# Optimization experiments

Hardware: AMD Instinct MI355X
Metric: run time of the kernel (lower is better)

## Reference

```python
import jax, jax.numpy as jnp
import numpy as np

HEADS = 12
DIM_HEAD = 64
WINDOW = 16
SHIFT = 1  # fixed stand-in for random.randint(0, window-1)
SCALE = DIM_HEAD ** -0.5


def window_cls_mask(n, window, shift):
    # Shifted block-diagonal mask over the n-1 non-CLS tokens, CLS attends/attended everywhere.
    size = n - 1
    idx = jnp.arange(size)
    cur = (idx - shift) % window
    left = jnp.clip(idx - cur, 0, size)
    right = jnp.clip(idx + (window - cur), 0, size)
    i = idx[:, None]  # query position
    wmask = (i >= left[None, :]) & (i < right[None, :])  # [size, size]
    full = jnp.ones((n, n), dtype=bool)
    full = full.at[1:, 1:].set(wmask)
    return full  # [n, n] bool


def setup_inputs() -> dict:
    key = jax.random.key(0)
    k1, k2, k3 = jax.random.split(key, 3)
    b, n, dim = 2, 2049, 768
    inner = HEADS * DIM_HEAD
    return {
        "x": jax.random.normal(k1, (b, n, dim), dtype=jnp.float32),
        "w_qkv": jax.random.normal(k2, (dim, 3 * inner), dtype=jnp.float32) * 0.02,
        "w_out": jax.random.normal(k3, (inner, dim), dtype=jnp.float32) * 0.02,
        "b_out": jnp.zeros((dim,), dtype=jnp.float32),
    }


def reference(x, w_qkv, w_out, b_out):
    b, n, dim = x.shape
    h, d = HEADS, DIM_HEAD
    qkv = x @ w_qkv  # [b, n, 3*h*d]
    q, k, v = jnp.split(qkv, 3, axis=-1)
    # b n (h d) -> b h n d
    reshape = lambda t: t.reshape(b, n, h, d).transpose(0, 2, 1, 3)
    q, k, v = reshape(q), reshape(k), reshape(v)
    dots = jnp.einsum('bhid,bhjd->bhij', q, k) * SCALE  # [b, h, n, n]
    mask = window_cls_mask(n, WINDOW, SHIFT)  # [n, n]
    neg = -jnp.finfo(dots.dtype).max
    dots = jnp.where(mask[None, None], dots, neg)
    attn = jax.nn.softmax(dots, axis=-1)
    out = jnp.einsum('bhij,bhjd->bhid', attn, v)  # [b, h, n, d]
    out = out.transpose(0, 2, 1, 3).reshape(b, n, h * d)
    return out @ w_out + b_out
```

## Files before the change

kernel.cpp:

```cpp
#include <hip/hip_runtime.h>
#include <hip/hip_bf16.h>
#include <math.h>

typedef __attribute__((ext_vector_type(8))) __bf16 bf16x8;
typedef __attribute__((ext_vector_type(4))) float f32x4;

#define HEADS 12
#define DHEAD 64
#define NTOK 2049
#define BATCH 2
#define DIM 768
#define QKV3 2304
#define MROWS 4098
#define MP 4224
#define ATT_SCALE 0.125f
#define BKS 64
#define NSPLIT 33
#define PSTRIDE 68

#define CVT_BLOCKS 1584
#define TQKV_BX 72
#define TQKV_BLOCKS (72 * 24)
#define TOUT_BX 24
#define TOUT_BLOCKS (24 * 24)
#define PREP_BLOCKS (CVT_BLOCKS + TQKV_BLOCKS + TOUT_BLOCKS)
#define WIN_BLOCKS (BATCH * 129 * 3)

__global__ __launch_bounds__(256) void prep_kernel(const float* __restrict__ x,
                                                   const float* __restrict__ w_qkv,
                                                   const float* __restrict__ w_out,
                                                   __bf16* __restrict__ xb,
                                                   __bf16* __restrict__ wqkvT,
                                                   __bf16* __restrict__ woutT) {
  __shared__ float tile[32][33];
  const int b = blockIdx.x, tid = threadIdx.x;
  if (b < CVT_BLOCKS) {
    long e = ((long)b * 256 + tid) * 8;
    int row = (int)(e / DIM);
    bf16x8 v;
    if (row < MROWS) {
      const float4 a = *(const float4*)(x + e);
      const float4 c = *(const float4*)(x + e + 4);
      v[0] = (__bf16)a.x; v[1] = (__bf16)a.y; v[2] = (__bf16)a.z; v[3] = (__bf16)a.w;
      v[4] = (__bf16)c.x; v[5] = (__bf16)c.y; v[6] = (__bf16)c.z; v[7] = (__bf16)c.w;
    } else {
#pragma unroll
      for (int j = 0; j < 8; ++j) v[j] = (__bf16)0.f;
    }
    *(bf16x8*)(xb + e) = v;
    return;
  }
  const float* in;
  __bf16* outp;
  int C, bx, by;
  if (b < CVT_BLOCKS + TQKV_BLOCKS) {
    int idx = b - CVT_BLOCKS;
    bx = idx % TQKV_BX; by = idx / TQKV_BX;
    in = w_qkv; outp = wqkvT; C = QKV3;
  } else {
    int idx = b - CVT_BLOCKS - TQKV_BLOCKS;
    bx = idx % TOUT_BX; by = idx / TOUT_BX;
    in = w_out; outp = woutT; C = DIM;
  }
  const int R = DIM;
  const int c0 = bx * 32, r0 = by * 32;
  const int tx = tid & 31, ty = tid >> 5;
#pragma unroll
  for (int i = 0; i < 4; ++i) {
    int r = ty + i * 8;
    tile[r][tx] = in[(size_t)(r0 + r) * C + c0 + tx];
  }
  __syncthreads();
#pragma unroll
  for (int i = 0; i < 4; ++i) {
    int r = ty + i * 8;
    outp[(size_t)(c0 + r) * R + r0 + tx] = (__bf16)tile[tx][r];
  }
}

template <bool BF16_OUT>
__global__ __launch_bounds__(256) void gemm128_kernel(const __bf16* __restrict__ A,
                                                      const __bf16* __restrict__ Bt,
                                                      void* __restrict__ Cv,
                                                      const float* __restrict__ bias,
                                                      int N, int K, int Mvalid) {
  __shared__ __bf16 sA[2][128 * BKS];
  __shared__ __bf16 sB[2][128 * BKS];
  const int tid = threadIdx.x;
  const int w = tid >> 6, lane = tid & 63;
  const int m0 = blockIdx.y * 128, n0 = blockIdx.x * 128;
  const int wr = w >> 1, wc = w & 1;
  f32x4 acc[4][4] = {};

  const int srow = (w << 5) + (lane >> 3);
  const int scol = ((lane & 7) ^ (lane >> 3)) << 3;
  const __bf16* gA = A + (size_t)(m0 + srow) * K + scol;
  const __bf16* gB = Bt + (size_t)(n0 + srow) * K + scol;
  const int ldsoff0 = (w << 2) << 9;

  const int nk = K / BKS;

#define STAGE(buf, kt)                                                                   \
  do {                                                                                   \
    _Pragma("unroll")                                                                    \
    for (int it = 0; it < 4; ++it) {                                                     \
      __builtin_amdgcn_global_load_lds(                                                  \
          (const __attribute__((address_space(1))) void*)(gA + (size_t)(it * 8) * K + (kt)), \
          (__attribute__((address_space(3))) void*)(&sA[buf][ldsoff0 + (it << 9)]), 16, 0, 0); \
      __builtin_amdgcn_global_load_lds(                                                  \
          (const __attribute__((address_space(1))) void*)(gB + (size_t)(it * 8) * K + (kt)), \
          (__attribute__((address_space(3))) void*)(&sB[buf][ldsoff0 + (it << 9)]), 16, 0, 0); \
    }                                                                                    \
  } while (0)

  STAGE(0, 0);
  __syncthreads();

  const int sw0 = ((lane >> 4) ^ (lane & 7)) << 3;
  const int sw1 = sw0 ^ 32;
  const int rofA = (wr * 64 + (lane & 15)) * BKS;
  const int rofB = (wc * 64 + (lane & 15)) * BKS;

  for (int t = 0; t < nk; ++t) {
    const int cur = t & 1;
    if (t + 1 < nk) STAGE(cur ^ 1, (t + 1) * BKS);
    const __bf16* bufA = sA[cur];
    const __bf16* bufB = sB[cur];
#pragma unroll
    for (int kk = 0; kk < BKS; kk += 32) {
      const int so = (kk == 0) ? sw0 : sw1;
      bf16x8 af[4], bfr[4];
#pragma unroll
      for (int m = 0; m < 4; ++m)
        af[m] = *(const bf16x8*)&bufA[rofA + m * 16 * BKS + so];
#pragma unroll
      for (int n = 0; n < 4; ++n)
        bfr[n] = *(const bf16x8*)&bufB[rofB + n * 16 * BKS + so];
#pragma unroll
      for (int m = 0; m < 4; ++m)
#pragma unroll
        for (int n = 0; n < 4; ++n)
          acc[m][n] = __builtin_amdgcn_mfma_f32_16x16x32_bf16(af[m], bfr[n], acc[m][n], 0, 0, 0);
    }
    __syncthreads();
  }
#undef STAGE

#pragma unroll
  for (int m = 0; m < 4; ++m) {
#pragma unroll
    for (int n = 0; n < 4; ++n) {
      int col = n0 + wc * 64 + n * 16 + (lane & 15);
      int rbase = m0 + wr * 64 + m * 16 + ((lane >> 4) << 2);
#pragma unroll
      for (int r = 0; r < 4; ++r) {
        int row = rbase + r;
        float val = acc[m][n][r];
        if constexpr (BF16_OUT) {
          ((__bf16*)Cv)[(size_t)row * N + col] = (__bf16)val;
        } else {
          if (row < Mvalid) ((float*)Cv)[(size_t)row * N + col] = val + bias[col];
        }
      }
    }
  }
}

__global__ __launch_bounds__(64) void attn_fused_kernel(const __bf16* __restrict__ qkv,
                                                        __bf16* __restrict__ attnb,
                                                        float* __restrict__ part) {
  __shared__ float sp_lds[64];
  const int lane = threadIdx.x;

  if (blockIdx.x < WIN_BLOCKS) {
    int bidx = blockIdx.x;
    int hg = bidx % 3; bidx /= 3;
    int blk = bidx % 129;
    int bb = bidx / 129;
    int h = hg * 4 + (lane >> 4);
    int qi = lane & 15;
    int t0 = (blk == 0) ? 1 : 2 + 16 * (blk - 1);
    int nt = (blk == 0) ? 1 : ((NTOK - t0) < 16 ? (NTOK - t0) : 16);
    bool active = qi < nt;
    int qt = t0 + (active ? qi : nt - 1);
    const size_t base = (size_t)bb * NTOK * QKV3;

    float q[64];
    {
      const __bf16* qp = qkv + base + (size_t)qt * QKV3 + h * DHEAD;
#pragma unroll
      for (int d0 = 0; d0 < 64; d0 += 8) {
        bf16x8 v = *(const bf16x8*)(qp + d0);
#pragma unroll
        for (int j = 0; j < 8; ++j) q[d0 + j] = (float)v[j];
      }
    }

    float s[17];
    float mx = -3.4e38f;
#pragma unroll
    for (int j = 0; j < 17; ++j) {
      int jc = (j - 1) < (nt - 1) ? (j - 1) : (nt - 1);
      int kt = (j == 0) ? 0 : t0 + jc;
      const __bf16* kp = qkv + base + (size_t)kt * QKV3 + DIM + h * DHEAD;
      float dot = 0.f;
#pragma unroll
      for (int d0 = 0; d0 < 64; d0 += 8) {
        bf16x8 v = *(const bf16x8*)(kp + d0);
#pragma unroll
        for (int jj = 0; jj < 8; ++jj) dot = fmaf(q[d0 + jj], (float)v[jj], dot);
      }
      s[j] = (j <= nt) ? dot * ATT_SCALE : -3.4e38f;
      mx = fmaxf(mx, s[j]);
    }
    float sum = 0.f;
#pragma unroll
    for (int j = 0; j < 17; ++j) {
      s[j] = expf(s[j] - mx);
      sum += s[j];
    }
    float inv = 1.f / sum;

    float o[64];
#pragma unroll
    for (int d = 0; d < 64; ++d) o[d] = 0.f;
#pragma unroll
    for (int j = 0; j < 17; ++j) {
      int jc = (j - 1) < (nt - 1) ? (j - 1) : (nt - 1);
      int vt = (j == 0) ? 0 : t0 + jc;
      const __bf16* vp = qkv + base + (size_t)vt * QKV3 + 2 * DIM + h * DHEAD;
      float p = s[j];
#pragma unroll
      for (int d0 = 0; d0 < 64; d0 += 8) {
        bf16x8 v = *(const bf16x8*)(vp + d0);
#pragma unroll
        for (int jj = 0; jj < 8; ++jj) o[d0 + jj] = fmaf(p, (float)v[jj], o[d0 + jj]);
      }
    }

    if (active) {
      __bf16* op = attnb + (size_t)(bb * NTOK + qt) * DIM + h * DHEAD;
#pragma unroll
      for (int d0 = 0; d0 < 64; d0 += 8) {
        bf16x8 v;
#pragma unroll
        for (int j = 0; j < 8; ++j) v[j] = (__bf16)(o[d0 + j] * inv);
        *(bf16x8*)(op + d0) = v;
      }
    }
    return;
  }

  int bid = blockIdx.x - WIN_BLOCKS;
  const int sp = bid % NSPLIT;
  const int bh = bid / NSPLIT;
  const int h = bh % HEADS;
  const int bb = bh / HEADS;
  const size_t base = (size_t)bb * NTOK * QKV3;

  float q[64];
  {
    const __bf16* qp = qkv + base + h * DHEAD;
#pragma unroll
    for (int d0 = 0; d0 < 64; d0 += 8) {
      bf16x8 v = *(const bf16x8*)(qp + d0);
#pragma unroll
      for (int j = 0; j < 8; ++j) q[d0 + j] = (float)v[j];
    }
  }

  const int t = sp * 64 + lane;
  const bool valid = t < NTOK;
  const int tc = valid ? t : NTOK - 1;
  float dot = 0.f;
  {
    const __bf16* kp = qkv + base + (size_t)tc * QKV3 + DIM + h * DHEAD;
#pragma unroll
    for (int d0 = 0; d0 < 64; d0 += 8) {
      bf16x8 v = *(const bf16x8*)(kp + d0);
#pragma unroll
      for (int j = 0; j < 8; ++j) dot = fmaf(q[d0 + j], (float)v[j], dot);
    }
  }
  float s = valid ? dot * ATT_SCALE : -3.4e38f;

  float m = s;
#pragma unroll
  for (int off = 32; off > 0; off >>= 1) m = fmaxf(m, __shfl_xor(m, off, 64));
  float p = valid ? expf(s - m) : 0.f;
  float l = p;
#pragma unroll
  for (int off = 32; off > 0; off >>= 1) l += __shfl_xor(l, off, 64);

  sp_lds[lane] = p;
  __syncthreads();

  const int nt = (NTOK - sp * 64) < 64 ? (NTOK - sp * 64) : 64;
  float o = 0.f;
  const __bf16* vcol = qkv + base + (size_t)(sp * 64) * QKV3 + 2 * DIM + h * DHEAD + lane;
  for (int tt = 0; tt < nt; ++tt) {
    o = fmaf(sp_lds[tt], (float)vcol[(size_t)tt * QKV3], o);
  }

  float* pb = part + ((size_t)bh * NSPLIT + sp) * PSTRIDE;
  pb[lane] = o;
  if (lane == 0) { pb[64] = m; pb[65] = l; }
}

__global__ __launch_bounds__(64) void attn_cls_reduce(const float* __restrict__ part,
                                                      __bf16* __restrict__ attnb) {
  const int bh = blockIdx.x;
  const int h = bh % HEADS;
  const int bb = bh / HEADS;
  const int lane = threadIdx.x;
  const float* pb0 = part + (size_t)bh * NSPLIT * PSTRIDE;
  float M = -3.4e38f;
#pragma unroll
  for (int i = 0; i < NSPLIT; ++i) M = fmaxf(M, pb0[i * PSTRIDE + 64]);
  float L = 0.f, o = 0.f;
#pragma unroll
  for (int i = 0; i < NSPLIT; ++i) {
    float w = expf(pb0[i * PSTRIDE + 64] - M);
    L = fmaf(pb0[i * PSTRIDE + 65], w, L);
    o = fmaf(pb0[i * PSTRIDE + lane], w, o);
  }
  attnb[(size_t)(bb * NTOK) * DIM + h * DHEAD + lane] = (__bf16)(o / L);
}

extern "C" void kernel_launch(void* const* d_in, const int* in_sizes, int n_in,
                              void* d_out, int out_size, void* d_ws, size_t ws_size,
                              hipStream_t stream) {
  const float* x = (const float*)d_in[0];
  const float* w_qkv = (const float*)d_in[1];
  const float* w_out = (const float*)d_in[2];
  const float* b_out = (const float*)d_in[3];
  float* out = (float*)d_out;

  char* ws = (char*)d_ws;
  __bf16* xb    = (__bf16*)(ws);
  __bf16* wqkvT = (__bf16*)(ws + 6488064);
  __bf16* woutT = (__bf16*)(ws + 6488064 + 3538944);
  __bf16* qkvb  = (__bf16*)(ws + 6488064 + 3538944 + 1179648);
  __bf16* attnb = (__bf16*)(ws + 6488064 + 3538944 + 1179648 + 19464192);
  float*  clsp  = (float*)(ws + 6488064 + 3538944 + 1179648 + 19464192 + 6488064);

  prep_kernel<<<PREP_BLOCKS, 256, 0, stream>>>(x, w_qkv, w_out, xb, wqkvT, woutT);

  gemm128_kernel<true><<<dim3(QKV3 / 128, MP / 128), 256, 0, stream>>>(
      xb, wqkvT, (void*)qkvb, nullptr, QKV3, DIM, MP);

  attn_fused_kernel<<<WIN_BLOCKS + BATCH * HEADS * NSPLIT, 64, 0, stream>>>(qkvb, attnb, clsp);
  attn_cls_reduce<<<BATCH * HEADS, 64, 0, stream>>>(clsp, attnb);

  gemm128_kernel<false><<<dim3(DIM / 128, MP / 128), 256, 0, stream>>>(
      attnb, woutT, (void*)out, b_out, DIM, DIM, MROWS);
}
```

Before: 156.6 us.

## Fuse fp32-to-bf16 conversion of x into the QKV GEMM A-tile load

Removes the separate conversion of x to bf16 in the prep kernel. The QKV GEMM now reads fp32 x directly into registers, converts it, and writes bf16 into LDS, with the next tile's global loads issued before the MFMA loop. This drops a full bf16 copy of x written to and read back from global memory. In exchange, A-tile staging moves from async global_load_lds to register loads plus LDS stores, which raises register pressure and reads twice as many bytes per A tile from global memory, since each tile is re-read by all 18 column blocks.

```diff
diff --git a/kernel.cpp b/kernel.cpp
--- a/kernel.cpp
+++ b/kernel.cpp
@@ -18,47 +18,27 @@
 #define NSPLIT 33
 #define PSTRIDE 68
 
-#define CVT_BLOCKS 1584
 #define TQKV_BX 72
 #define TQKV_BLOCKS (72 * 24)
 #define TOUT_BX 24
 #define TOUT_BLOCKS (24 * 24)
-#define PREP_BLOCKS (CVT_BLOCKS + TQKV_BLOCKS + TOUT_BLOCKS)
+#define PREP_BLOCKS (TQKV_BLOCKS + TOUT_BLOCKS)
 #define WIN_BLOCKS (BATCH * 129 * 3)
 
-__global__ __launch_bounds__(256) void prep_kernel(const float* __restrict__ x,
-                                                   const float* __restrict__ w_qkv,
+__global__ __launch_bounds__(256) void prep_kernel(const float* __restrict__ w_qkv,
                                                    const float* __restrict__ w_out,
-                                                   __bf16* __restrict__ xb,
                                                    __bf16* __restrict__ wqkvT,
                                                    __bf16* __restrict__ woutT) {
   __shared__ float tile[32][33];
   const int b = blockIdx.x, tid = threadIdx.x;
-  if (b < CVT_BLOCKS) {
-    long e = ((long)b * 256 + tid) * 8;
-    int row = (int)(e / DIM);
-    bf16x8 v;
-    if (row < MROWS) {
-      const float4 a = *(const float4*)(x + e);
-      const float4 c = *(const float4*)(x + e + 4);
-      v[0] = (__bf16)a.x; v[1] = (__bf16)a.y; v[2] = (__bf16)a.z; v[3] = (__bf16)a.w;
-      v[4] = (__bf16)c.x; v[5] = (__bf16)c.y; v[6] = (__bf16)c.z; v[7] = (__bf16)c.w;
-    } else {
-#pragma unroll
-      for (int j = 0; j < 8; ++j) v[j] = (__bf16)0.f;
-    }
-    *(bf16x8*)(xb + e) = v;
-    return;
-  }
   const float* in;
   __bf16* outp;
   int C, bx, by;
-  if (b < CVT_BLOCKS + TQKV_BLOCKS) {
-    int idx = b - CVT_BLOCKS;
-    bx = idx % TQKV_BX; by = idx / TQKV_BX;
+  if (b < TQKV_BLOCKS) {
+    bx = b % TQKV_BX; by = b / TQKV_BX;
     in = w_qkv; outp = wqkvT; C = QKV3;
   } else {
-    int idx = b - CVT_BLOCKS - TQKV_BLOCKS;
+    int idx = b - TQKV_BLOCKS;
     bx = idx % TOUT_BX; by = idx / TOUT_BX;
     in = w_out; outp = woutT; C = DIM;
   }
@@ -78,12 +58,9 @@
   }
 }
 
-template <bool BF16_OUT>
-__global__ __launch_bounds__(256) void gemm128_kernel(const __bf16* __restrict__ A,
-                                                      const __bf16* __restrict__ Bt,
-                                                      void* __restrict__ Cv,
-                                                      const float* __restrict__ bias,
-                                                      int N, int K, int Mvalid) {
+__global__ __launch_bounds__(256) void gemm_qkv_kernel(const float* __restrict__ X,
+                                                       const __bf16* __restrict__ Bt,
+                                                       __bf16* __restrict__ C) {
   __shared__ __bf16 sA[2][128 * BKS];
   __shared__ __bf16 sB[2][128 * BKS];
   const int tid = threadIdx.x;
@@ -93,11 +70,126 @@
   f32x4 acc[4][4] = {};
 
   const int srow = (w << 5) + (lane >> 3);
+  const int scolE = ((lane & 7) ^ (lane >> 3)) << 3;
+  const __bf16* gB = Bt + (size_t)(n0 + srow) * DIM + scolE;
+  const int ldsoff0 = (w << 2) << 9;
+
+  const int nk = DIM / BKS;
+  float4 av[4][2];
+
+#define LOAD_A(kt)                                                              \
+  do {                                                                          \
+    _Pragma("unroll")                                                           \
+    for (int it = 0; it < 4; ++it) {                                            \
+      int row = m0 + srow + it * 8;                                             \
+      if (row < MROWS) {                                                        \
+        const float* gp = X + (size_t)row * DIM + (kt) + scolE;                 \
+        av[it][0] = *(const float4*)gp;                                         \
+        av[it][1] = *(const float4*)(gp + 4);                                   \
+      } else {                                                                  \
+        av[it][0] = make_float4(0.f, 0.f, 0.f, 0.f);                            \
+        av[it][1] = make_float4(0.f, 0.f, 0.f, 0.f);                            \
+      }                                                                         \
+    }                                                                           \
+  } while (0)
+
+#define WRITE_A(buf)                                                            \
+  do {                                                                          \
+    _Pragma("unroll")                                                           \
+    for (int it = 0; it < 4; ++it) {                                            \
+      bf16x8 v;                                                                 \
+      _Pragma("unroll")                                                         \
+      for (int j = 0; j < 4; ++j) {                                             \
+        v[j] = (__bf16)((&av[it][0].x)[j]);                                     \
+        v[4 + j] = (__bf16)((&av[it][1].x)[j]);                                 \
+      }                                                                         \
+      *(bf16x8*)&sA[buf][ldsoff0 + (it << 9) + lane * 8] = v;                   \
+    }                                                                           \
+  } while (0)
+
+#define STAGE_B(buf, kt)                                                                 \
+  do {                                                                                   \
+    _Pragma("unroll")                                                                    \
+    for (int it = 0; it < 4; ++it) {                                                     \
+      __builtin_amdgcn_global_load_lds(                                                  \
+          (const __attribute__((address_space(1))) void*)(gB + (size_t)(it * 8) * DIM + (kt)), \
+          (__attribute__((address_space(3))) void*)(&sB[buf][ldsoff0 + (it << 9)]), 16, 0, 0); \
+    }                                                                                    \
+  } while (0)
+
+  LOAD_A(0);
+  STAGE_B(0, 0);
+  WRITE_A(0);
+  __syncthreads();
+
+  const int sw0 = ((lane >> 4) ^ (lane & 7)) << 3;
+  const int sw1 = sw0 ^ 32;
+  const int rofA = (wr * 64 + (lane & 15)) * BKS;
+  const int rofB = (wc * 64 + (lane & 15)) * BKS;
+
+  for (int t = 0; t < nk; ++t) {
+    const int cur = t & 1, nx = cur ^ 1;
+    if (t + 1 < nk) {
+      STAGE_B(nx, (t + 1) * BKS);
+      LOAD_A((t + 1) * BKS);
+    }
+    const __bf16* bufA = sA[cur];
+    const __bf16* bufB = sB[cur];
+#pragma unroll
+    for (int kk = 0; kk < BKS; kk += 32) {
+      const int so = (kk == 0) ? sw0 : sw1;
+      bf16x8 af[4], bfr[4];
+#pragma unroll
+      for (int m = 0; m < 4; ++m)
+        af[m] = *(const bf16x8*)&bufA[rofA + m * 16 * BKS + so];
+#pragma unroll
+      for (int n = 0; n < 4; ++n)
+        bfr[n] = *(const bf16x8*)&bufB[rofB + n * 16 * BKS + so];
+#pragma unroll
+      for (int m = 0; m < 4; ++m)
+#pragma unroll
+        for (int n = 0; n < 4; ++n)
+          acc[m][n] = __builtin_amdgcn_mfma_f32_16x16x32_bf16(af[m], bfr[n], acc[m][n], 0, 0, 0);
+    }
+    if (t + 1 < nk) WRITE_A(nx);
+    __syncthreads();
+  }
+#undef LOAD_A
+#undef WRITE_A
+#undef STAGE_B
+
+#pragma unroll
+  for (int m = 0; m < 4; ++m) {
+#pragma unroll
+    for (int n = 0; n < 4; ++n) {
+      int col = n0 + wc * 64 + n * 16 + (lane & 15);
+      int rbase = m0 + wr * 64 + m * 16 + ((lane >> 4) << 2);
+#pragma unroll
+      for (int r = 0; r < 4; ++r) {
+        C[(size_t)(rbase + r) * QKV3 + col] = (__bf16)acc[m][n][r];
+      }
+    }
+  }
+}
+
+__global__ __launch_bounds__(256) void gemm_out_kernel(const __bf16* __restrict__ A,
+                                                       const __bf16* __restrict__ Bt,
+                                                       float* __restrict__ Cv,
+                                                       const float* __restrict__ bias) {
+  __shared__ __bf16 sA[2][128 * BKS];
+  __shared__ __bf16 sB[2][128 * BKS];
+  const int tid = threadIdx.x;
+  const int w = tid >> 6, lane = tid & 63;
+  const int m0 = blockIdx.y * 128, n0 = blockIdx.x * 128;
+  const int wr = w >> 1, wc = w & 1;
+  const int K = DIM, N = DIM;
+  f32x4 acc[4][4] = {};
+
+  const int srow = (w << 5) + (lane >> 3);
   const int scol = ((lane & 7) ^ (lane >> 3)) << 3;
   const __bf16* gA = A + (size_t)(m0 + srow) * K + scol;
   const __bf16* gB = Bt + (size_t)(n0 + srow) * K + scol;
   const int ldsoff0 = (w << 2) << 9;
-
   const int nk = K / BKS;
 
 #define STAGE(buf, kt)                                                                   \
@@ -155,12 +247,7 @@
 #pragma unroll
       for (int r = 0; r < 4; ++r) {
         int row = rbase + r;
-        float val = acc[m][n][r];
-        if constexpr (BF16_OUT) {
-          ((__bf16*)Cv)[(size_t)row * N + col] = (__bf16)val;
-        } else {
-          if (row < Mvalid) ((float*)Cv)[(size_t)row * N + col] = val + bias[col];
-        }
+        if (row < MROWS) Cv[(size_t)row * N + col] = acc[m][n][r] + bias[col];
       }
     }
   }
@@ -337,21 +424,18 @@
   float* out = (float*)d_out;
 
   char* ws = (char*)d_ws;
-  __bf16* xb    = (__bf16*)(ws);
-  __bf16* wqkvT = (__bf16*)(ws + 6488064);
-  __bf16* woutT = (__bf16*)(ws + 6488064 + 3538944);
-  __bf16* qkvb  = (__bf16*)(ws + 6488064 + 3538944 + 1179648);
-  __bf16* attnb = (__bf16*)(ws + 6488064 + 3538944 + 1179648 + 19464192);
-  float*  clsp  = (float*)(ws + 6488064 + 3538944 + 1179648 + 19464192 + 6488064);
-
-  prep_kernel<<<PREP_BLOCKS, 256, 0, stream>>>(x, w_qkv, w_out, xb, wqkvT, woutT);
-
-  gemm128_kernel<true><<<dim3(QKV3 / 128, MP / 128), 256, 0, stream>>>(
-      xb, wqkvT, (void*)qkvb, nullptr, QKV3, DIM, MP);
+  __bf16* wqkvT = (__bf16*)(ws);
+  __bf16* woutT = (__bf16*)(ws + 3538944);
+  __bf16* qkvb  = (__bf16*)(ws + 3538944 + 1179648);
+  __bf16* attnb = (__bf16*)(ws + 3538944 + 1179648 + 19464192);
+  float*  clsp  = (float*)(ws + 3538944 + 1179648 + 19464192 + 6488064);
+
+  prep_kernel<<<PREP_BLOCKS, 256, 0, stream>>>(w_qkv, w_out, wqkvT, woutT);
+
+  gemm_qkv_kernel<<<dim3(QKV3 / 128, MP / 128), 256, 0, stream>>>(x, wqkvT, qkvb);
 
   attn_fused_kernel<<<WIN_BLOCKS + BATCH * HEADS * NSPLIT, 64, 0, stream>>>(qkvb, attnb, clsp);
   attn_cls_reduce<<<BATCH * HEADS, 64, 0, stream>>>(clsp, attnb);
 
-  gemm128_kernel<false><<<dim3(DIM / 128, MP / 128), 256, 0, stream>>>(
-      attnb, woutT, (void*)out, b_out, DIM, DIM, MROWS);
-}
+  gemm_out_kernel<<<dim3(DIM / 128, MP / 128), 256, 0, stream>>>(attnb, woutT, out, b_out);
+}
```

Measured after the change: 177.2 us. 1.13x slower.
